# Kernel tuning notes

Measured on AMD Instinct MI355X. Metric: run time of the kernel, lower is better.

Reference implementation:

```python
import jax, jax.numpy as jnp
import numpy as np

H = 64  # hidden_size

def _gru_layer(x_seq, Wih, Whh, bih, bhh):
    """PyTorch-semantics GRU layer. x_seq: [B, T, D] -> [B, T, H].
    Gate order in weights is (r, z, n), matching nn.GRU."""
    B = x_seq.shape[0]
    # Precompute input projections for all timesteps at once: [B, T, 3H]
    x_proj = jnp.einsum('btd,gd->btg', x_seq, Wih) + bih
    x_proj = jnp.swapaxes(x_proj, 0, 1)  # [T, B, 3H] for scan

    def step(h, xp):
        hp = h @ Whh.T + bhh                      # [B, 3H]
        xr, xz, xn = jnp.split(xp, 3, axis=-1)
        hr, hz, hn = jnp.split(hp, 3, axis=-1)
        r = jax.nn.sigmoid(xr + hr)
        z = jax.nn.sigmoid(xz + hz)
        n = jnp.tanh(xn + r * hn)
        h_new = (1.0 - z) * n + z * h
        return h_new, h_new

    h0 = jnp.zeros((B, H), dtype=x_seq.dtype)
    _, hs = jax.lax.scan(step, h0, x_proj)        # hs: [T, B, H]
    return jnp.swapaxes(hs, 0, 1)                 # [B, T, H]


def setup_inputs() -> dict:
    key = jax.random.key(0)
    ks = jax.random.split(key, 12)
    B, T, D, O = 2048, 512, 1, 1
    s = 1.0 / np.sqrt(H)  # PyTorch GRU init scale
    return {
        'x':     jax.random.normal(ks[0], (B, T, D), jnp.float32),
        'W_ih0': jax.random.normal(ks[1], (3 * H, D), jnp.float32) * s,
        'W_hh0': jax.random.normal(ks[2], (3 * H, H), jnp.float32) * s,
        'b_ih0': jax.random.normal(ks[3], (3 * H,), jnp.float32) * s,
        'b_hh0': jax.random.normal(ks[4], (3 * H,), jnp.float32) * s,
        'W_ih1': jax.random.normal(ks[5], (3 * H, H), jnp.float32) * s,
        'W_hh1': jax.random.normal(ks[6], (3 * H, H), jnp.float32) * s,
        'b_ih1': jax.random.normal(ks[7], (3 * H,), jnp.float32) * s,
        'b_hh1': jax.random.normal(ks[8], (3 * H,), jnp.float32) * s,
        'W_fc':  jax.random.normal(ks[9], (O, H), jnp.float32) * s,
        'b_fc':  jax.random.normal(ks[10], (O,), jnp.float32) * s,
    }


def reference(x, W_ih0, W_hh0, b_ih0, b_hh0, W_ih1, W_hh1, b_ih1, b_hh1, W_fc, b_fc):
    h1 = _gru_layer(x, W_ih0, W_hh0, b_ih0, b_hh0)   # [B, T, H]
    h2 = _gru_layer(h1, W_ih1, W_hh1, b_ih1, b_hh1)  # [B, T, H]
    last = h2[:, -1, :]                              # [B, H]
    return last @ W_fc.T + b_fc                      # [B, O]
```

## Files before the change

### kernel.cpp

```cpp
#include <hip/hip_runtime.h>
#include <hip/hip_fp16.h>


#define T_LEN 512
#define ROWS  8
#define XPAD  513
#define LOG2E 1.44269504088896f

typedef float          f32x4 __attribute__((ext_vector_type(4)));
typedef __bf16         bf16x8 __attribute__((ext_vector_type(8)));
typedef unsigned short us8   __attribute__((ext_vector_type(8)));
typedef unsigned short ushort_t;

__device__ __forceinline__ float bf2f(ushort_t b){
    unsigned int u = ((unsigned int)b) << 16;
    return __uint_as_float(u);
}
__device__ __forceinline__ ushort_t f2bf(float f){
    unsigned int u = __float_as_uint(f);
    u = (u + 0x7FFFu + ((u >> 16) & 1u)) >> 16;
    return (ushort_t)u;
}
__device__ __forceinline__ float ld_any(const void* p, int i, bool f32){
    return f32 ? ((const float*)p)[i] : bf2f(((const ushort_t*)p)[i]);
}
__device__ __forceinline__ float exp2_fast(float x){
#if __has_builtin(__builtin_amdgcn_exp2f)
    return __builtin_amdgcn_exp2f(x);
#else
    return __expf(0.6931471805599453f * x);
#endif
}
__device__ __forceinline__ float sigm2(float t){
    return __fdividef(1.0f, 1.0f + exp2_fast(-t));
}
__device__ __forceinline__ float tanh2(float t){
    return fmaf(-2.0f, __fdividef(1.0f, exp2_fast(t) + 1.0f), 1.0f);
}
__device__ __forceinline__ f32x4 mfma16(bf16x8 a, bf16x8 b, f32x4 c){
    return __builtin_amdgcn_mfma_f32_16x16x32_bf16(a, b, c, 0, 0, 0);
}
__device__ __forceinline__ bf16x8 mk_frag(const void* W, int n, int kb, bool f32, float sc){
    us8 tmp;
    #pragma unroll
    for (int j = 0; j < 8; ++j){
        float v = f32 ? ((const float*)W)[n * 64 + kb + j]
                      : bf2f(((const ushort_t*)W)[n * 64 + kb + j]);
        tmp[j] = f2bf(v * sc);
    }
    return __builtin_bit_cast(bf16x8, tmp);
}

__global__ __launch_bounds__(512, 2) void gru_fused(
    const void* __restrict__ xv,
    const void* __restrict__ Wih0, const void* __restrict__ Whh0,
    const void* __restrict__ bih0, const void* __restrict__ bhh0,
    const void* __restrict__ Wih1, const void* __restrict__ Whh1,
    const void* __restrict__ bih1, const void* __restrict__ bhh1,
    const void* __restrict__ Wfc,  const void* __restrict__ bfc,
    void* __restrict__ outv)
{
    __shared__ float    xbuf[ROWS * XPAD];
    __shared__ ushort_t hbufA[2][16 * 72];
    __shared__ ushort_t hbufB[2][16 * 72];
    __shared__ float    outb[ROWS][68];

    const int tid  = threadIdx.x;
    const int wv   = tid >> 6;
    const bool isL1 = (wv >= 4);
    const int w    = wv & 3;
    const int c    = tid & 15;
    const int q    = (tid >> 4) & 3;
    const int ih   = w * 16 + c;
    const int r0   = 2 * q;
    const int m0   = 4 * q;
    const long row0 = (long)blockIdx.x * ROWS;

    bool f32 = false;
    {
        const ushort_t* xs = (const ushort_t*)xv;
        for (int j = 0; j < 64; ++j){
            int e = (xs[2 * j] >> 7) & 0xFF;
            if (e > 150) f32 = true;
        }
    }

    {
        ushort_t* pa = &hbufA[0][0];
        ushort_t* pb = &hbufB[0][0];
        for (int k = tid; k < 2 * 16 * 72; k += 512){ pa[k] = 0; pb[k] = 0; }
    }
    {
        const int r = wv;
        const int g = tid & 63;
        if (f32){
            const f32x4* src = (const f32x4*)((const float*)xv + (row0 + r) * T_LEN);
            #pragma unroll
            for (int it = 0; it < 2; ++it){
                f32x4 v = src[g + 64 * it];
                #pragma unroll
                for (int j = 0; j < 4; ++j)
                    xbuf[r * XPAD + (g + 64 * it) * 4 + j] = v[j];
            }
        } else {
            const us8* src = (const us8*)((const ushort_t*)xv + (row0 + r) * T_LEN);
            us8 v = src[g];
            #pragma unroll
            for (int j = 0; j < 8; ++j)
                xbuf[r * XPAD + g * 8 + j] = bf2f(v[j]);
        }
    }

    bf16x8 wA[3][2], wB[3][2];
    float sxr = 0.f, sxz = 0.f, sxn = 0.f;
    float br, bz, bnx, bnh;
    const float gsc0 = LOG2E, gsc2 = 2.0f * LOG2E;
    if (!isL1){
        #pragma unroll
        for (int g = 0; g < 3; ++g){
            const int n = g * 64 + ih;
            const float sc = (g == 2) ? gsc2 : gsc0;
            #pragma unroll
            for (int f = 0; f < 2; ++f)
                wA[g][f] = mk_frag(Whh0, n, f * 32 + q * 8, f32, sc);
        }
        sxr = ld_any(Wih0, ih, f32) * gsc0;
        sxz = ld_any(Wih0, 64 + ih, f32) * gsc0;
        sxn = ld_any(Wih0, 128 + ih, f32) * gsc2;
        br  = (ld_any(bih0, ih, f32)      + ld_any(bhh0, ih, f32))      * gsc0;
        bz  = (ld_any(bih0, 64 + ih, f32) + ld_any(bhh0, 64 + ih, f32)) * gsc0;
        bnx = ld_any(bih0, 128 + ih, f32) * gsc2;
        bnh = ld_any(bhh0, 128 + ih, f32) * gsc2;
    } else {
        #pragma unroll
        for (int g = 0; g < 3; ++g){
            const int n = g * 64 + ih;
            const float sc = (g == 2) ? gsc2 : gsc0;
            #pragma unroll
            for (int f = 0; f < 2; ++f){
                wA[g][f] = mk_frag(Wih1, n, f * 32 + q * 8, f32, sc);
                wB[g][f] = mk_frag(Whh1, n, f * 32 + q * 8, f32, sc);
            }
        }
        br  = (ld_any(bih1, ih, f32)      + ld_any(bhh1, ih, f32))      * gsc0;
        bz  = (ld_any(bih1, 64 + ih, f32) + ld_any(bhh1, 64 + ih, f32)) * gsc0;
        bnx = ld_any(bih1, 128 + ih, f32) * gsc2;
        bnh = ld_any(bhh1, 128 + ih, f32) * gsc2;
    }

    float h2[2] = {0.f, 0.f};
    const int aoff = c * 72 + q * 8;

    __syncthreads();

    for (int t = 0; t < T_LEN; ++t){
        const int p = t & 1;
        if (!isL1){
            us8 a0u = *(const us8*)&hbufA[p][aoff];
            us8 a1u = *(const us8*)&hbufA[p][aoff + 32];
            bf16x8 a0 = __builtin_bit_cast(bf16x8, a0u);
            bf16x8 a1 = __builtin_bit_cast(bf16x8, a1u);
            f32x4 aR = {br, br, br, br};
            f32x4 aZ = {bz, bz, bz, bz};
            f32x4 aN = {bnh, bnh, bnh, bnh};
            aR = mfma16(a0, wA[0][0], aR); aR = mfma16(a1, wA[0][1], aR);
            aZ = mfma16(a0, wA[1][0], aZ); aZ = mfma16(a1, wA[1][1], aZ);
            aN = mfma16(a0, wA[2][0], aN); aN = mfma16(a1, wA[2][1], aN);
            float xm[2] = { xbuf[r0 * XPAD + t], xbuf[(r0 + 1) * XPAD + t] };
            #pragma unroll
            for (int j = 0; j < 2; ++j){
                float rg = sigm2(fmaf(xm[j], sxr, aR[j]));
                float zg = sigm2(fmaf(xm[j], sxz, aZ[j]));
                float ng = tanh2(fmaf(xm[j], sxn, bnx) + rg * aN[j]);
                h2[j] = ng + zg * (h2[j] - ng);
                hbufA[p ^ 1][(m0 + j) * 72 + ih] = f2bf(h2[j]);
            }
        } else if (t > 0){
            us8 a0u = *(const us8*)&hbufA[p][aoff];
            us8 a1u = *(const us8*)&hbufA[p][aoff + 32];
            us8 b0u = *(const us8*)&hbufB[p][aoff];
            us8 b1u = *(const us8*)&hbufB[p][aoff + 32];
            bf16x8 a0 = __builtin_bit_cast(bf16x8, a0u);
            bf16x8 a1 = __builtin_bit_cast(bf16x8, a1u);
            bf16x8 b0 = __builtin_bit_cast(bf16x8, b0u);
            bf16x8 b1 = __builtin_bit_cast(bf16x8, b1u);
            f32x4 aR  = {br, br, br, br};
            f32x4 aZ  = {bz, bz, bz, bz};
            f32x4 aXn = {bnx, bnx, bnx, bnx};
            f32x4 aHn = {bnh, bnh, bnh, bnh};
            aR  = mfma16(a0, wA[0][0], aR);  aR  = mfma16(a1, wA[0][1], aR);
            aR  = mfma16(b0, wB[0][0], aR);  aR  = mfma16(b1, wB[0][1], aR);
            aZ  = mfma16(a0, wA[1][0], aZ);  aZ  = mfma16(a1, wA[1][1], aZ);
            aZ  = mfma16(b0, wB[1][0], aZ);  aZ  = mfma16(b1, wB[1][1], aZ);
            aXn = mfma16(a0, wA[2][0], aXn); aXn = mfma16(a1, wA[2][1], aXn);
            aHn = mfma16(b0, wB[2][0], aHn); aHn = mfma16(b1, wB[2][1], aHn);
            #pragma unroll
            for (int j = 0; j < 2; ++j){
                float rg = sigm2(aR[j]);
                float zg = sigm2(aZ[j]);
                float ng = tanh2(aXn[j] + rg * aHn[j]);
                h2[j] = ng + zg * (h2[j] - ng);
                hbufB[p ^ 1][(m0 + j) * 72 + ih] = f2bf(h2[j]);
            }
        }
        __syncthreads();
    }

    if (isL1){
        us8 a0u = *(const us8*)&hbufA[0][aoff];
        us8 a1u = *(const us8*)&hbufA[0][aoff + 32];
        us8 b0u = *(const us8*)&hbufB[0][aoff];
        us8 b1u = *(const us8*)&hbufB[0][aoff + 32];
        bf16x8 a0 = __builtin_bit_cast(bf16x8, a0u);
        bf16x8 a1 = __builtin_bit_cast(bf16x8, a1u);
        bf16x8 b0 = __builtin_bit_cast(bf16x8, b0u);
        bf16x8 b1 = __builtin_bit_cast(bf16x8, b1u);
        f32x4 aR  = {br, br, br, br};
        f32x4 aZ  = {bz, bz, bz, bz};
        f32x4 aXn = {bnx, bnx, bnx, bnx};
        f32x4 aHn = {bnh, bnh, bnh, bnh};
        aR  = mfma16(a0, wA[0][0], aR);  aR  = mfma16(a1, wA[0][1], aR);
        aR  = mfma16(b0, wB[0][0], aR);  aR  = mfma16(b1, wB[0][1], aR);
        aZ  = mfma16(a0, wA[1][0], aZ);  aZ  = mfma16(a1, wA[1][1], aZ);
        aZ  = mfma16(b0, wB[1][0], aZ);  aZ  = mfma16(b1, wB[1][1], aZ);
        aXn = mfma16(a0, wA[2][0], aXn); aXn = mfma16(a1, wA[2][1], aXn);
        aHn = mfma16(b0, wB[2][0], aHn); aHn = mfma16(b1, wB[2][1], aHn);
        #pragma unroll
        for (int j = 0; j < 2; ++j){
            float rg = sigm2(aR[j]);
            float zg = sigm2(aZ[j]);
            float ng = tanh2(aXn[j] + rg * aHn[j]);
            float hf = ng + zg * (h2[j] - ng);
            outb[r0 + j][ih] = hf;
        }
    }
    __syncthreads();

    if (tid < ROWS){
        float s = ld_any(bfc, 0, f32);
        for (int i2 = 0; i2 < 64; ++i2) s = fmaf(ld_any(Wfc, i2, f32), outb[tid][i2], s);
        if (f32) ((float*)outv)[row0 + tid] = s;
        else     ((ushort_t*)outv)[row0 + tid] = f2bf(s);
    }
}

extern "C" void kernel_launch(void* const* d_in, const int* in_sizes, int n_in,
                              void* d_out, int out_size, void* d_ws, size_t ws_size,
                              hipStream_t stream)
{
    (void)in_sizes; (void)n_in; (void)d_ws; (void)ws_size;
    const int B = out_size;
    const int nblk = B / ROWS;
    gru_fused<<<nblk, 512, 0, stream>>>(
        d_in[0],
        d_in[1], d_in[2], d_in[3], d_in[4],
        d_in[5], d_in[6], d_in[7], d_in[8],
        d_in[9], d_in[10],
        d_out);
}
```

Baseline: 392.7 us.

## Restructure GRU kernel to one wave per layer with register-resident hidden state

Each block now handles 16 batch rows with two waves, one per layer. Each wave computes all 64 hidden units through transposed MFMAs, so the hidden state stays in registers as the B operand and no LDS round-trip is needed within a layer. Only layer 0's output is passed through LDS, and the final FC reduction uses shuffles. It also swaps division for hardware rcp and uses packed bf16 conversion. The cost is fewer threads per block and heavy register pressure per wave, which may limit latency hiding.

```diff
diff --git a/kernel.cpp b/kernel.cpp
--- a/kernel.cpp
+++ b/kernel.cpp
@@ -1,15 +1,15 @@
 #include <hip/hip_runtime.h>
-#include <hip/hip_fp16.h>
 
 
 #define T_LEN 512
-#define ROWS  8
+#define BROWS 16
 #define XPAD  513
 #define LOG2E 1.44269504088896f
 
 typedef float          f32x4 __attribute__((ext_vector_type(4)));
 typedef __bf16         bf16x8 __attribute__((ext_vector_type(8)));
 typedef unsigned short us8   __attribute__((ext_vector_type(8)));
+typedef unsigned int   ui4   __attribute__((ext_vector_type(4)));
 typedef unsigned short ushort_t;
 
 __device__ __forceinline__ float bf2f(ushort_t b){
@@ -31,14 +31,26 @@
     return __expf(0.6931471805599453f * x);
 #endif
 }
+__device__ __forceinline__ float rcp_fast(float x){
+#if __has_builtin(__builtin_amdgcn_rcpf)
+    return __builtin_amdgcn_rcpf(x);
+#else
+    return __fdividef(1.0f, x);
+#endif
+}
 __device__ __forceinline__ float sigm2(float t){
-    return __fdividef(1.0f, 1.0f + exp2_fast(-t));
+    return rcp_fast(1.0f + exp2_fast(-t));
 }
 __device__ __forceinline__ float tanh2(float t){
-    return fmaf(-2.0f, __fdividef(1.0f, exp2_fast(t) + 1.0f), 1.0f);
+    return fmaf(-2.0f, rcp_fast(exp2_fast(t) + 1.0f), 1.0f);
 }
 __device__ __forceinline__ f32x4 mfma16(bf16x8 a, bf16x8 b, f32x4 c){
     return __builtin_amdgcn_mfma_f32_16x16x32_bf16(a, b, c, 0, 0, 0);
+}
+__device__ __forceinline__ unsigned int cvtpk(float lo, float hi){
+    unsigned int r;
+    asm("v_cvt_pk_bf16_f32 %0, %1, %2" : "=v"(r) : "v"(lo), "v"(hi));
+    return r;
 }
 __device__ __forceinline__ bf16x8 mk_frag(const void* W, int n, int kb, bool f32, float sc){
     us8 tmp;
@@ -51,7 +63,7 @@
     return __builtin_bit_cast(bf16x8, tmp);
 }
 
-__global__ __launch_bounds__(512, 2) void gru_fused(
+__global__ __launch_bounds__(128, 1) void gru_fused(
     const void* __restrict__ xv,
     const void* __restrict__ Wih0, const void* __restrict__ Whh0,
     const void* __restrict__ bih0, const void* __restrict__ bhh0,
@@ -60,21 +72,16 @@
     const void* __restrict__ Wfc,  const void* __restrict__ bfc,
     void* __restrict__ outv)
 {
-    __shared__ float    xbuf[ROWS * XPAD];
-    __shared__ ushort_t hbufA[2][16 * 72];
-    __shared__ ushort_t hbufB[2][16 * 72];
-    __shared__ float    outb[ROWS][68];
-
-    const int tid  = threadIdx.x;
-    const int wv   = tid >> 6;
-    const bool isL1 = (wv >= 4);
-    const int w    = wv & 3;
-    const int c    = tid & 15;
-    const int q    = (tid >> 4) & 3;
-    const int ih   = w * 16 + c;
-    const int r0   = 2 * q;
-    const int m0   = 4 * q;
-    const long row0 = (long)blockIdx.x * ROWS;
+    __shared__ float xbuf[BROWS * XPAD];
+    __shared__ ui4   hAx[2][64][2];
+
+    const int tid = threadIdx.x;
+    const int wv  = tid >> 6;
+    const int l   = tid & 63;
+    const int b   = l & 15;
+    const int hp  = l >> 4;
+    const int am  = l & 15;
+    const long row0 = (long)blockIdx.x * BROWS;
 
     bool f32 = false;
     {
@@ -85,162 +92,190 @@
         }
     }
 
-    {
-        ushort_t* pa = &hbufA[0][0];
-        ushort_t* pb = &hbufB[0][0];
-        for (int k = tid; k < 2 * 16 * 72; k += 512){ pa[k] = 0; pb[k] = 0; }
-    }
-    {
-        const int r = wv;
-        const int g = tid & 63;
-        if (f32){
-            const f32x4* src = (const f32x4*)((const float*)xv + (row0 + r) * T_LEN);
-            #pragma unroll
-            for (int it = 0; it < 2; ++it){
-                f32x4 v = src[g + 64 * it];
-                #pragma unroll
-                for (int j = 0; j < 4; ++j)
-                    xbuf[r * XPAD + (g + 64 * it) * 4 + j] = v[j];
-            }
-        } else {
-            const us8* src = (const us8*)((const ushort_t*)xv + (row0 + r) * T_LEN);
-            us8 v = src[g];
-            #pragma unroll
-            for (int j = 0; j < 8; ++j)
-                xbuf[r * XPAD + g * 8 + j] = bf2f(v[j]);
-        }
-    }
-
-    bf16x8 wA[3][2], wB[3][2];
-    float sxr = 0.f, sxz = 0.f, sxn = 0.f;
-    float br, bz, bnx, bnh;
+    if (f32){
+        for (int idx = tid; idx < BROWS * (T_LEN / 4); idx += 128){
+            const int r = idx >> 7, sg = idx & 127;
+            f32x4 v = ((const f32x4*)((const float*)xv + (row0 + r) * T_LEN))[sg];
+            #pragma unroll
+            for (int j = 0; j < 4; ++j) xbuf[r * XPAD + sg * 4 + j] = v[j];
+        }
+    } else {
+        for (int idx = tid; idx < BROWS * (T_LEN / 8); idx += 128){
+            const int r = idx >> 6, sg = idx & 63;
+            us8 v = ((const us8*)((const ushort_t*)xv + (row0 + r) * T_LEN))[sg];
+            #pragma unroll
+            for (int j = 0; j < 8; ++j) xbuf[r * XPAD + sg * 8 + j] = bf2f(v[j]);
+        }
+    }
+
     const float gsc0 = LOG2E, gsc2 = 2.0f * LOG2E;
-    if (!isL1){
+
+    ui4 z4 = {0u, 0u, 0u, 0u};
+    bf16x8 sf0 = __builtin_bit_cast(bf16x8, z4);
+    bf16x8 sf1 = sf0;
+    f32x4 hS[4] = {{0,0,0,0},{0,0,0,0},{0,0,0,0},{0,0,0,0}};
+
+    if (wv == 0){
+        bf16x8 wh[3][4][2];
+        f32x4 cbR[4], cbZ[4], cbNx[4], cbNh[4];
+        f32x4 cwR[4], cwZ[4], cwN[4];
         #pragma unroll
         for (int g = 0; g < 3; ++g){
-            const int n = g * 64 + ih;
             const float sc = (g == 2) ? gsc2 : gsc0;
             #pragma unroll
-            for (int f = 0; f < 2; ++f)
-                wA[g][f] = mk_frag(Whh0, n, f * 32 + q * 8, f32, sc);
-        }
-        sxr = ld_any(Wih0, ih, f32) * gsc0;
-        sxz = ld_any(Wih0, 64 + ih, f32) * gsc0;
-        sxn = ld_any(Wih0, 128 + ih, f32) * gsc2;
-        br  = (ld_any(bih0, ih, f32)      + ld_any(bhh0, ih, f32))      * gsc0;
-        bz  = (ld_any(bih0, 64 + ih, f32) + ld_any(bhh0, 64 + ih, f32)) * gsc0;
-        bnx = ld_any(bih0, 128 + ih, f32) * gsc2;
-        bnh = ld_any(bhh0, 128 + ih, f32) * gsc2;
+            for (int tau = 0; tau < 4; ++tau){
+                const int grow = g * 64 + 32 * (tau >> 1) + 8 * (am >> 2)
+                               + 4 * (tau & 1) + (am & 3);
+                wh[g][tau][0] = mk_frag(Whh0, grow, 8 * hp,      f32, sc);
+                wh[g][tau][1] = mk_frag(Whh0, grow, 32 + 8 * hp, f32, sc);
+            }
+        }
+        #pragma unroll
+        for (int tau = 0; tau < 4; ++tau){
+            #pragma unroll
+            for (int r = 0; r < 4; ++r){
+                const int hc = 32 * (tau >> 1) + 8 * hp + 4 * (tau & 1) + r;
+                cbR[tau][r]  = (ld_any(bih0, hc, f32) + ld_any(bhh0, hc, f32)) * gsc0;
+                cwR[tau][r]  = ld_any(Wih0, hc, f32) * gsc0;
+                cbZ[tau][r]  = (ld_any(bih0, 64 + hc, f32) + ld_any(bhh0, 64 + hc, f32)) * gsc0;
+                cwZ[tau][r]  = ld_any(Wih0, 64 + hc, f32) * gsc0;
+                cbNx[tau][r] = ld_any(bih0, 128 + hc, f32) * gsc2;
+                cbNh[tau][r] = ld_any(bhh0, 128 + hc, f32) * gsc2;
+                cwN[tau][r]  = ld_any(Wih0, 128 + hc, f32) * gsc2;
+            }
+        }
+        __syncthreads();
+
+        for (int t = 0; t < T_LEN; ++t){
+            const float xb = xbuf[b * XPAD + t];
+            f32x4 aR[4], aZ[4], aN[4], aX[4];
+            #pragma unroll
+            for (int tau = 0; tau < 4; ++tau){
+                #pragma unroll
+                for (int r = 0; r < 4; ++r){
+                    aR[tau][r] = fmaf(xb, cwR[tau][r], cbR[tau][r]);
+                    aZ[tau][r] = fmaf(xb, cwZ[tau][r], cbZ[tau][r]);
+                    aX[tau][r] = fmaf(xb, cwN[tau][r], cbNx[tau][r]);
+                }
+            }
+            #pragma unroll
+            for (int tau = 0; tau < 4; ++tau){
+                aR[tau] = mfma16(wh[0][tau][0], sf0, aR[tau]);
+                aR[tau] = mfma16(wh[0][tau][1], sf1, aR[tau]);
+                aZ[tau] = mfma16(wh[1][tau][0], sf0, aZ[tau]);
+                aZ[tau] = mfma16(wh[1][tau][1], sf1, aZ[tau]);
+                aN[tau] = mfma16(wh[2][tau][0], sf0, cbNh[tau]);
+                aN[tau] = mfma16(wh[2][tau][1], sf1, aN[tau]);
+            }
+            unsigned int w[8];
+            #pragma unroll
+            for (int tau = 0; tau < 4; ++tau){
+                #pragma unroll
+                for (int r = 0; r < 4; ++r){
+                    float rg = sigm2(aR[tau][r]);
+                    float zg = sigm2(aZ[tau][r]);
+                    float ng = tanh2(aX[tau][r] + rg * aN[tau][r]);
+                    hS[tau][r] = ng + zg * (hS[tau][r] - ng);
+                }
+                w[2 * tau]     = cvtpk(hS[tau][0], hS[tau][1]);
+                w[2 * tau + 1] = cvtpk(hS[tau][2], hS[tau][3]);
+            }
+            ui4 q0 = {w[0], w[1], w[2], w[3]};
+            ui4 q1 = {w[4], w[5], w[6], w[7]};
+            sf0 = __builtin_bit_cast(bf16x8, q0);
+            sf1 = __builtin_bit_cast(bf16x8, q1);
+            hAx[t & 1][l][0] = q0;
+            hAx[t & 1][l][1] = q1;
+            __syncthreads();
+        }
     } else {
+        bf16x8 wi[3][4][2], wh[3][4][2];
+        f32x4 cbR[4], cbZ[4], cbNx[4], cbNh[4];
         #pragma unroll
         for (int g = 0; g < 3; ++g){
-            const int n = g * 64 + ih;
             const float sc = (g == 2) ? gsc2 : gsc0;
             #pragma unroll
-            for (int f = 0; f < 2; ++f){
-                wA[g][f] = mk_frag(Wih1, n, f * 32 + q * 8, f32, sc);
-                wB[g][f] = mk_frag(Whh1, n, f * 32 + q * 8, f32, sc);
-            }
-        }
-        br  = (ld_any(bih1, ih, f32)      + ld_any(bhh1, ih, f32))      * gsc0;
-        bz  = (ld_any(bih1, 64 + ih, f32) + ld_any(bhh1, 64 + ih, f32)) * gsc0;
-        bnx = ld_any(bih1, 128 + ih, f32) * gsc2;
-        bnh = ld_any(bhh1, 128 + ih, f32) * gsc2;
-    }
-
-    float h2[2] = {0.f, 0.f};
-    const int aoff = c * 72 + q * 8;
-
-    __syncthreads();
-
-    for (int t = 0; t < T_LEN; ++t){
-        const int p = t & 1;
-        if (!isL1){
-            us8 a0u = *(const us8*)&hbufA[p][aoff];
-            us8 a1u = *(const us8*)&hbufA[p][aoff + 32];
-            bf16x8 a0 = __builtin_bit_cast(bf16x8, a0u);
-            bf16x8 a1 = __builtin_bit_cast(bf16x8, a1u);
-            f32x4 aR = {br, br, br, br};
-            f32x4 aZ = {bz, bz, bz, bz};
-            f32x4 aN = {bnh, bnh, bnh, bnh};
-            aR = mfma16(a0, wA[0][0], aR); aR = mfma16(a1, wA[0][1], aR);
-            aZ = mfma16(a0, wA[1][0], aZ); aZ = mfma16(a1, wA[1][1], aZ);
-            aN = mfma16(a0, wA[2][0], aN); aN = mfma16(a1, wA[2][1], aN);
-            float xm[2] = { xbuf[r0 * XPAD + t], xbuf[(r0 + 1) * XPAD + t] };
-            #pragma unroll
-            for (int j = 0; j < 2; ++j){
-                float rg = sigm2(fmaf(xm[j], sxr, aR[j]));
-                float zg = sigm2(fmaf(xm[j], sxz, aZ[j]));
-                float ng = tanh2(fmaf(xm[j], sxn, bnx) + rg * aN[j]);
-                h2[j] = ng + zg * (h2[j] - ng);
-                hbufA[p ^ 1][(m0 + j) * 72 + ih] = f2bf(h2[j]);
-            }
-        } else if (t > 0){
-            us8 a0u = *(const us8*)&hbufA[p][aoff];
-            us8 a1u = *(const us8*)&hbufA[p][aoff + 32];
-            us8 b0u = *(const us8*)&hbufB[p][aoff];
-            us8 b1u = *(const us8*)&hbufB[p][aoff + 32];
-            bf16x8 a0 = __builtin_bit_cast(bf16x8, a0u);
-            bf16x8 a1 = __builtin_bit_cast(bf16x8, a1u);
-            bf16x8 b0 = __builtin_bit_cast(bf16x8, b0u);
-            bf16x8 b1 = __builtin_bit_cast(bf16x8, b1u);
-            f32x4 aR  = {br, br, br, br};
-            f32x4 aZ  = {bz, bz, bz, bz};
-            f32x4 aXn = {bnx, bnx, bnx, bnx};
-            f32x4 aHn = {bnh, bnh, bnh, bnh};
-            aR  = mfma16(a0, wA[0][0], aR);  aR  = mfma16(a1, wA[0][1], aR);
-            aR  = mfma16(b0, wB[0][0], aR);  aR  = mfma16(b1, wB[0][1], aR);
-            aZ  = mfma16(a0, wA[1][0], aZ);  aZ  = mfma16(a1, wA[1][1], aZ);
-            aZ  = mfma16(b0, wB[1][0], aZ);  aZ  = mfma16(b1, wB[1][1], aZ);
-            aXn = mfma16(a0, wA[2][0], aXn); aXn = mfma16(a1, wA[2][1], aXn);
-            aHn = mfma16(b0, wB[2][0], aHn); aHn = mfma16(b1, wB[2][1], aHn);
-            #pragma unroll
-            for (int j = 0; j < 2; ++j){
-                float rg = sigm2(aR[j]);
-                float zg = sigm2(aZ[j]);
-                float ng = tanh2(aXn[j] + rg * aHn[j]);
-                h2[j] = ng + zg * (h2[j] - ng);
-                hbufB[p ^ 1][(m0 + j) * 72 + ih] = f2bf(h2[j]);
+            for (int tau = 0; tau < 4; ++tau){
+                const int grow = g * 64 + 32 * (tau >> 1) + 8 * (am >> 2)
+                               + 4 * (tau & 1) + (am & 3);
+                wi[g][tau][0] = mk_frag(Wih1, grow, 8 * hp,      f32, sc);
+                wi[g][tau][1] = mk_frag(Wih1, grow, 32 + 8 * hp, f32, sc);
+                wh[g][tau][0] = mk_frag(Whh1, grow, 8 * hp,      f32, sc);
+                wh[g][tau][1] = mk_frag(Whh1, grow, 32 + 8 * hp, f32, sc);
+            }
+        }
+        #pragma unroll
+        for (int tau = 0; tau < 4; ++tau){
+            #pragma unroll
+            for (int r = 0; r < 4; ++r){
+                const int hc = 32 * (tau >> 1) + 8 * hp + 4 * (tau & 1) + r;
+                cbR[tau][r]  = (ld_any(bih1, hc, f32) + ld_any(bhh1, hc, f32)) * gsc0;
+                cbZ[tau][r]  = (ld_any(bih1, 64 + hc, f32) + ld_any(bhh1, 64 + hc, f32)) * gsc0;
+                cbNx[tau][r] = ld_any(bih1, 128 + hc, f32) * gsc2;
+                cbNh[tau][r] = ld_any(bhh1, 128 + hc, f32) * gsc2;
             }
         }
         __syncthreads();
-    }
-
-    if (isL1){
-        us8 a0u = *(const us8*)&hbufA[0][aoff];
-        us8 a1u = *(const us8*)&hbufA[0][aoff + 32];
-        us8 b0u = *(const us8*)&hbufB[0][aoff];
-        us8 b1u = *(const us8*)&hbufB[0][aoff + 32];
-        bf16x8 a0 = __builtin_bit_cast(bf16x8, a0u);
-        bf16x8 a1 = __builtin_bit_cast(bf16x8, a1u);
-        bf16x8 b0 = __builtin_bit_cast(bf16x8, b0u);
-        bf16x8 b1 = __builtin_bit_cast(bf16x8, b1u);
-        f32x4 aR  = {br, br, br, br};
-        f32x4 aZ  = {bz, bz, bz, bz};
-        f32x4 aXn = {bnx, bnx, bnx, bnx};
-        f32x4 aHn = {bnh, bnh, bnh, bnh};
-        aR  = mfma16(a0, wA[0][0], aR);  aR  = mfma16(a1, wA[0][1], aR);
-        aR  = mfma16(b0, wB[0][0], aR);  aR  = mfma16(b1, wB[0][1], aR);
-        aZ  = mfma16(a0, wA[1][0], aZ);  aZ  = mfma16(a1, wA[1][1], aZ);
-        aZ  = mfma16(b0, wB[1][0], aZ);  aZ  = mfma16(b1, wB[1][1], aZ);
-        aXn = mfma16(a0, wA[2][0], aXn); aXn = mfma16(a1, wA[2][1], aXn);
-        aHn = mfma16(b0, wB[2][0], aHn); aHn = mfma16(b1, wB[2][1], aHn);
-        #pragma unroll
-        for (int j = 0; j < 2; ++j){
-            float rg = sigm2(aR[j]);
-            float zg = sigm2(aZ[j]);
-            float ng = tanh2(aXn[j] + rg * aHn[j]);
-            float hf = ng + zg * (h2[j] - ng);
-            outb[r0 + j][ih] = hf;
-        }
-    }
-    __syncthreads();
-
-    if (tid < ROWS){
-        float s = ld_any(bfc, 0, f32);
-        for (int i2 = 0; i2 < 64; ++i2) s = fmaf(ld_any(Wfc, i2, f32), outb[tid][i2], s);
-        if (f32) ((float*)outv)[row0 + tid] = s;
-        else     ((ushort_t*)outv)[row0 + tid] = f2bf(s);
+
+        for (int t = 0; t <= T_LEN; ++t){
+            if (t > 0){
+                ui4 q0 = hAx[(t - 1) & 1][l][0];
+                ui4 q1 = hAx[(t - 1) & 1][l][1];
+                bf16x8 gA0 = __builtin_bit_cast(bf16x8, q0);
+                bf16x8 gA1 = __builtin_bit_cast(bf16x8, q1);
+                f32x4 aR[4], aZ[4], aX[4], aN[4];
+                #pragma unroll
+                for (int tau = 0; tau < 4; ++tau){
+                    aR[tau] = mfma16(wi[0][tau][0], gA0, cbR[tau]);
+                    aR[tau] = mfma16(wi[0][tau][1], gA1, aR[tau]);
+                    aR[tau] = mfma16(wh[0][tau][0], sf0, aR[tau]);
+                    aR[tau] = mfma16(wh[0][tau][1], sf1, aR[tau]);
+                    aZ[tau] = mfma16(wi[1][tau][0], gA0, cbZ[tau]);
+                    aZ[tau] = mfma16(wi[1][tau][1], gA1, aZ[tau]);
+                    aZ[tau] = mfma16(wh[1][tau][0], sf0, aZ[tau]);
+                    aZ[tau] = mfma16(wh[1][tau][1], sf1, aZ[tau]);
+                    aX[tau] = mfma16(wi[2][tau][0], gA0, cbNx[tau]);
+                    aX[tau] = mfma16(wi[2][tau][1], gA1, aX[tau]);
+                    aN[tau] = mfma16(wh[2][tau][0], sf0, cbNh[tau]);
+                    aN[tau] = mfma16(wh[2][tau][1], sf1, aN[tau]);
+                }
+                unsigned int w[8];
+                #pragma unroll
+                for (int tau = 0; tau < 4; ++tau){
+                    #pragma unroll
+                    for (int r = 0; r < 4; ++r){
+                        float rg = sigm2(aR[tau][r]);
+                        float zg = sigm2(aZ[tau][r]);
+                        float ng = tanh2(aX[tau][r] + rg * aN[tau][r]);
+                        hS[tau][r] = ng + zg * (hS[tau][r] - ng);
+                    }
+                    w[2 * tau]     = cvtpk(hS[tau][0], hS[tau][1]);
+                    w[2 * tau + 1] = cvtpk(hS[tau][2], hS[tau][3]);
+                }
+                ui4 p0 = {w[0], w[1], w[2], w[3]};
+                ui4 p1 = {w[4], w[5], w[6], w[7]};
+                sf0 = __builtin_bit_cast(bf16x8, p0);
+                sf1 = __builtin_bit_cast(bf16x8, p1);
+            }
+            if (t < T_LEN) __syncthreads();
+        }
+
+        float part = 0.0f;
+        #pragma unroll
+        for (int tau = 0; tau < 4; ++tau){
+            #pragma unroll
+            for (int r = 0; r < 4; ++r){
+                const int hc = 32 * (tau >> 1) + 8 * hp + 4 * (tau & 1) + r;
+                part = fmaf(ld_any(Wfc, hc, f32), hS[tau][r], part);
+            }
+        }
+        part += __shfl_xor(part, 16);
+        part += __shfl_xor(part, 32);
+        if (l < 16){
+            float s = part + ld_any(bfc, 0, f32);
+            if (f32) ((float*)outv)[row0 + b] = s;
+            else     ((ushort_t*)outv)[row0 + b] = f2bf(s);
+        }
     }
 }
 
@@ -250,8 +285,8 @@
 {
     (void)in_sizes; (void)n_in; (void)d_ws; (void)ws_size;
     const int B = out_size;
-    const int nblk = B / ROWS;
-    gru_fused<<<nblk, 512, 0, stream>>>(
+    const int nblk = B / BROWS;
+    gru_fused<<<nblk, 128, 0, stream>>>(
         d_in[0],
         d_in[1], d_in[2], d_in[3], d_in[4],
         d_in[5], d_in[6], d_in[7], d_in[8],
```

New measurement: 628.0 us. +59.9%, slower.
